# Performance work log

Measured on AMD Instinct MI355X. Metric: run time of the kernel, lower is better.

Reference implementation:

```python
import jax, jax.numpy as jnp
import numpy as np

N_NODES = 100000
N_EDGES = 3200000
NUM_GRAPHS = 2048
IN_CH = 35
HID = 128
EPS = 1e-5


def setup_inputs() -> dict:
    key = jax.random.key(0)
    ks = jax.random.split(key, 16)
    x = jax.random.normal(ks[0], (N_NODES, IN_CH), dtype=jnp.float32)
    edge_index = jax.random.randint(ks[1], (2, N_EDGES), 0, N_NODES, dtype=jnp.int64)
    batch = jnp.sort(jax.random.randint(ks[2], (N_NODES,), 0, NUM_GRAPHS, dtype=jnp.int64))
    def lin(k, fan_in, fan_out):
        b = 1.0 / np.sqrt(fan_in)
        kw, kb = jax.random.split(k)
        W = jax.random.uniform(kw, (fan_in, fan_out), minval=-b, maxval=b, dtype=jnp.float32)
        bias = jax.random.uniform(kb, (fan_out,), minval=-b, maxval=b, dtype=jnp.float32)
        return W, bias
    W1, b1 = lin(ks[3], IN_CH, HID)
    W2, b2 = lin(ks[4], HID, HID)
    W3, b3 = lin(ks[5], HID, HID)
    Wl1, bl1 = lin(ks[6], HID, HID // 2)
    Wl2, bl2 = lin(ks[7], HID // 2, 1)
    ones = jnp.ones((HID,), jnp.float32)
    zeros = jnp.zeros((HID,), jnp.float32)
    return {
        'x': x, 'edge_index': edge_index, 'batch': batch,
        'W1': W1, 'b1': b1, 'g1': ones, 'be1': zeros,
        'W2': W2, 'b2': b2, 'g2': ones, 'be2': zeros,
        'W3': W3, 'b3': b3, 'g3': ones, 'be3': zeros,
        'Wl1': Wl1, 'bl1': bl1, 'Wl2': Wl2, 'bl2': bl2,
    }


def _gcn_norm(edge_index, n):
    # add self-loops, compute symmetric normalization D^-1/2 (A+I) D^-1/2
    loop = jnp.arange(n, dtype=edge_index.dtype)
    src = jnp.concatenate([edge_index[0], loop])
    dst = jnp.concatenate([edge_index[1], loop])
    deg = jax.ops.segment_sum(jnp.ones_like(dst, jnp.float32), dst, num_segments=n)
    dinv = jnp.where(deg > 0, jax.lax.rsqrt(deg), 0.0)
    norm = dinv[src] * dinv[dst]
    return src, dst, norm


def _gcn_conv(x, src, dst, norm, W, b):
    h = x @ W                      # [N, out]
    msg = h[src] * norm[:, None]   # gather + scale (irregular)
    out = jax.ops.segment_sum(msg, dst, num_segments=x.shape[0])
    return out + b


def _bn(x, g, be):
    mu = jnp.mean(x, axis=0)
    var = jnp.mean(jnp.square(x - mu), axis=0)  # biased var (torch BN training)
    return (x - mu) * jax.lax.rsqrt(var + EPS) * g + be


def reference(x, edge_index, batch, W1, b1, g1, be1, W2, b2, g2, be2,
              W3, b3, g3, be3, Wl1, bl1, Wl2, bl2):
    n = x.shape[0]
    src, dst, norm = _gcn_norm(edge_index, n)
    h = jax.nn.gelu(_bn(_gcn_conv(x, src, dst, norm, W1, b1), g1, be1), approximate=False)
    h = jax.nn.gelu(_bn(_gcn_conv(h, src, dst, norm, W2, b2), g2, be2), approximate=False)
    h = jax.nn.gelu(_bn(_gcn_conv(h, src, dst, norm, W3, b3), g3, be3), approximate=False)
    # global mean pool by graph id
    s = jax.ops.segment_sum(h, batch, num_segments=NUM_GRAPHS)
    cnt = jax.ops.segment_sum(jnp.ones((n,), jnp.float32), batch, num_segments=NUM_GRAPHS)
    pooled = s / jnp.maximum(cnt, 1.0)[:, None]
    out = jax.nn.elu(pooled @ Wl1 + bl1)
    out = out @ Wl2 + bl2
    return out  # [NUM_GRAPHS, 1]
```

## Files before the change

### kernel.cpp

```cpp
#include <hip/hip_runtime.h>
#include <hip/hip_bf16.h>
#include <math.h>

#define N_NODES 100000
#define N_EDGES 3200000
#define NUM_GRAPHS 2048
#define IN_CH 35
#define HID 128
#define BN_EPS 1e-5f

#define BUCK_SHIFT 9
#define BUCK_SIZE 512
#define NB_BUCK 196
#define BUCK_CAP 18432
#define BIN_GRID 1024
#define BIN_CHUNK 3128

typedef short bf16x8 __attribute__((ext_vector_type(8)));
typedef float f32x4 __attribute__((ext_vector_type(4)));

__device__ __forceinline__ float gelu_f(float x) {
    return 0.5f * x * (1.0f + erff(x * 0.70710678118654752440f));
}

__device__ __forceinline__ float bflo(unsigned v) { return __uint_as_float(v << 16); }
__device__ __forceinline__ float bfhi(unsigned v) { return __uint_as_float(v & 0xffff0000u); }
__device__ __forceinline__ unsigned f2bf(float f) {
    unsigned x = __float_as_uint(f);
    return (x + 0x7fffu + ((x >> 16) & 1u)) >> 16;
}
__device__ __forceinline__ unsigned packbf2(float lo, float hi) {
    return f2bf(lo) | (f2bf(hi) << 16);
}


__global__ void k_zero2(int* __restrict__ gcnt, float* __restrict__ stats,
                        unsigned* __restrict__ xzero, unsigned* __restrict__ hzero) {
    int i = threadIdx.x;
    if (i < NB_BUCK) gcnt[i] = 0;
    if (i < 3 * 256) stats[i] = 0.0f;
    if (i < 32) xzero[i] = 0u;
    if (i < 64) hzero[i] = 0u;
}


__global__ void k_wcast(const float* __restrict__ W2, const float* __restrict__ W3,
                        unsigned* __restrict__ Wt2, unsigned* __restrict__ Wt3) {
    int t = blockIdx.x * 256 + threadIdx.x;
    if (t >= 2 * 8192) return;
    const float* W = (t < 8192) ? W2 : W3;
    unsigned* Wt = (t < 8192) ? Wt2 : Wt3;
    int i = t & 8191;
    int n = i >> 6, j = i & 63;
    Wt[n * 64 + j] = packbf2(W[(2 * j) * HID + n], W[(2 * j + 1) * HID + n]);
}


__global__ void k_bin(const int* __restrict__ ei, int* __restrict__ gcnt,
                      unsigned* __restrict__ epack) {
    __shared__ unsigned lpack[BIN_CHUNK];
    __shared__ unsigned char lbuck[BIN_CHUNK];
    __shared__ int hist[NB_BUCK];
    __shared__ int hbase[NB_BUCK];
    __shared__ int lcur[NB_BUCK];
    int tid = threadIdx.x;
    if (tid < NB_BUCK) { hist[tid] = 0; lcur[tid] = 0; }
    __syncthreads();
    int e0 = blockIdx.x * BIN_CHUNK;
    int nE = min(e0 + BIN_CHUNK, N_EDGES) - e0;
    for (int i = tid * 4; i < nE; i += 1024) {
        int4 s4 = *(const int4*)(ei + e0 + i);
        int4 d4 = *(const int4*)(ei + N_EDGES + e0 + i);
        lpack[i + 0] = (unsigned)s4.x | (((unsigned)d4.x & 511u) << 17);
        lpack[i + 1] = (unsigned)s4.y | (((unsigned)d4.y & 511u) << 17);
        lpack[i + 2] = (unsigned)s4.z | (((unsigned)d4.z & 511u) << 17);
        lpack[i + 3] = (unsigned)s4.w | (((unsigned)d4.w & 511u) << 17);
        int b0 = d4.x >> BUCK_SHIFT, b1 = d4.y >> BUCK_SHIFT;
        int b2 = d4.z >> BUCK_SHIFT, b3 = d4.w >> BUCK_SHIFT;
        lbuck[i + 0] = (unsigned char)b0;
        lbuck[i + 1] = (unsigned char)b1;
        lbuck[i + 2] = (unsigned char)b2;
        lbuck[i + 3] = (unsigned char)b3;
        atomicAdd(&hist[b0], 1);
        atomicAdd(&hist[b1], 1);
        atomicAdd(&hist[b2], 1);
        atomicAdd(&hist[b3], 1);
    }
    __syncthreads();
    if (tid < NB_BUCK) {
        int h = hist[tid];
        hbase[tid] = (h > 0) ? (tid * BUCK_CAP + atomicAdd(&gcnt[tid], h)) : 0;
    }
    __syncthreads();
    for (int i = tid; i < nE; i += 256) {
        int b = lbuck[i];
        int off = atomicAdd(&lcur[b], 1);
        epack[hbase[b] + off] = lpack[i];
    }
}


__global__ void k_fill(const int* __restrict__ gcnt, const unsigned* __restrict__ epack,
                       int* __restrict__ rowp, int* __restrict__ rowpEnd,
                       float* __restrict__ dinv, int* __restrict__ col) {
    __shared__ int ldeg[BUCK_SIZE];
    __shared__ int sa[BUCK_SIZE];
    __shared__ int sb[BUCK_SIZE];
    __shared__ int lcur[BUCK_SIZE];
    int b = blockIdx.x;
    int tid = threadIdx.x;
    int base_node = b << BUCK_SHIFT;
    int nn = min(BUCK_SIZE, N_NODES - base_node);
    int seg0 = b * BUCK_CAP;
    int seg1 = seg0 + gcnt[b];
    ldeg[tid] = 0;
    __syncthreads();
    for (int e = seg0 + tid; e < seg1; e += BUCK_SIZE) {
        atomicAdd(&ldeg[epack[e] >> 17], 1);
    }
    __syncthreads();
    sa[tid] = ldeg[tid];
    __syncthreads();
    int* src = sa; int* dst = sb;
    for (int st = 1; st < BUCK_SIZE; st <<= 1) {
        int v = src[tid];
        if (tid >= st) v += src[tid - st];
        dst[tid] = v;
        __syncthreads();
        int* t = src; src = dst; dst = t;
    }
    int ex = (tid == 0) ? 0 : src[tid - 1];
    int rp = seg0 + ex;
    lcur[tid] = rp;
    if (tid < nn) {
        rowp[base_node + tid] = rp;
        rowpEnd[base_node + tid] = rp + ldeg[tid];
        dinv[base_node + tid] = rsqrtf((float)(ldeg[tid] + 1));
    }
    __syncthreads();
    for (int e = seg0 + tid; e < seg1; e += BUCK_SIZE) {
        unsigned v = epack[e];
        int p = atomicAdd(&lcur[v >> 17], 1);
        col[p] = (int)(v & 0x1FFFFu);
    }
}


__global__ void k_castx(const float* __restrict__ X, const float* __restrict__ dinv,
                        unsigned* __restrict__ Xb) {
    int i = blockIdx.x * blockDim.x + threadIdx.x;
    if (i >= N_NODES * 32) return;
    int n = i >> 5, j = i & 31;
    float dv = dinv[n];
    float lo = 0.0f, hi = 0.0f;
    if (j < 17) {
        lo = X[(size_t)n * IN_CH + 2 * j];
        hi = X[(size_t)n * IN_CH + 2 * j + 1];
    } else if (j == 17) {
        lo = X[(size_t)n * IN_CH + 34];
    }
    Xb[i] = packbf2(dv * lo, dv * hi);
}

#define ACC8(v) { a0 += bflo(v.x); a1 += bfhi(v.x); a2 += bflo(v.y); a3 += bfhi(v.y); \
                  a4 += bflo(v.z); a5 += bfhi(v.z); a6 += bflo(v.w); a7 += bfhi(v.w); }
#define ACC4(v) { a0 += bflo(v.x); a1 += bfhi(v.x); a2 += bflo(v.y); a3 += bfhi(v.y); }


#define C1_NODES 8

__global__ __launch_bounds__(512) void k_conv1(
        const unsigned* __restrict__ Xb, const int* __restrict__ rowp,
        const int* __restrict__ rowpEnd, const int* __restrict__ col,
        const float* __restrict__ dinv,
        const float* __restrict__ W1, const float* __restrict__ b1,
        unsigned* __restrict__ Yb) {
    __shared__ float w_s[IN_CH * HID];
    __shared__ float b_s[HID];
    __shared__ float xa_s[C1_NODES][36];
    int tid = threadIdx.x;
    for (int u = tid; u < IN_CH * HID; u += 512) w_s[u] = W1[u];
    if (tid < HID) b_s[tid] = b1[tid];

    int wid = tid >> 6;
    int lane = tid & 63;
    int g = lane >> 4;
    int j = lane & 15;
    int node = blockIdx.x * C1_NODES + wid;
    bool valid = node < N_NODES;

    float a0 = 0.0f, a1 = 0.0f, a2 = 0.0f, a3 = 0.0f;
    float di = 0.0f;
    if (valid) {
        int rp0 = rowp[node], rp1 = rowpEnd[node];
        di = dinv[node];
        uint2 sv = *(const uint2*)(Xb + (size_t)node * 32 + j * 2);
        float w0 = (g == 0) ? 1.0f : 0.0f;
        a0 = w0 * bflo(sv.x); a1 = w0 * bfhi(sv.x);
        a2 = w0 * bflo(sv.y); a3 = w0 * bfhi(sv.y);
        unsigned deg = (unsigned)(rp1 - rp0);
        for (int e0 = (rp0 & ~3); e0 < rp1; e0 += 32) {
            int ebA = e0 + 4 * g;
            int ebB = ebA + 16;
            int4 cA = *(const int4*)(col + ebA);
            int4 cB = *(const int4*)(col + ebB);
            int s0 = ((unsigned)(ebA + 0 - rp0) < deg) ? cA.x : N_NODES;
            int s1 = ((unsigned)(ebA + 1 - rp0) < deg) ? cA.y : N_NODES;
            int s2 = ((unsigned)(ebA + 2 - rp0) < deg) ? cA.z : N_NODES;
            int s3 = ((unsigned)(ebA + 3 - rp0) < deg) ? cA.w : N_NODES;
            int s4 = ((unsigned)(ebB + 0 - rp0) < deg) ? cB.x : N_NODES;
            int s5 = ((unsigned)(ebB + 1 - rp0) < deg) ? cB.y : N_NODES;
            int s6 = ((unsigned)(ebB + 2 - rp0) < deg) ? cB.z : N_NODES;
            int s7 = ((unsigned)(ebB + 3 - rp0) < deg) ? cB.w : N_NODES;
            uint2 v0 = *(const uint2*)(Xb + (size_t)s0 * 32 + j * 2);
            uint2 v1 = *(const uint2*)(Xb + (size_t)s1 * 32 + j * 2);
            uint2 v2 = *(const uint2*)(Xb + (size_t)s2 * 32 + j * 2);
            uint2 v3 = *(const uint2*)(Xb + (size_t)s3 * 32 + j * 2);
            uint2 v4 = *(const uint2*)(Xb + (size_t)s4 * 32 + j * 2);
            uint2 v5 = *(const uint2*)(Xb + (size_t)s5 * 32 + j * 2);
            uint2 v6 = *(const uint2*)(Xb + (size_t)s6 * 32 + j * 2);
            uint2 v7 = *(const uint2*)(Xb + (size_t)s7 * 32 + j * 2);
            ACC4(v0); ACC4(v1); ACC4(v2); ACC4(v3);
            ACC4(v4); ACC4(v5); ACC4(v6); ACC4(v7);
        }
    }
    a0 += __shfl(a0, (lane + 32) & 63, 64);
    a1 += __shfl(a1, (lane + 32) & 63, 64);
    a2 += __shfl(a2, (lane + 32) & 63, 64);
    a3 += __shfl(a3, (lane + 32) & 63, 64);
    a0 += __shfl(a0, (lane + 16) & 63, 64);
    a1 += __shfl(a1, (lane + 16) & 63, 64);
    a2 += __shfl(a2, (lane + 16) & 63, 64);
    a3 += __shfl(a3, (lane + 16) & 63, 64);
    if (valid && g == 0 && j < 9) {
        xa_s[wid][4 * j + 0] = di * a0;
        xa_s[wid][4 * j + 1] = di * a1;
        xa_s[wid][4 * j + 2] = di * a2;
        xa_s[wid][4 * j + 3] = di * a3;
    }
    __syncthreads();
    float acc0 = b_s[2 * lane];
    float acc1 = b_s[2 * lane + 1];
    #pragma unroll 7
    for (int k = 0; k < IN_CH; ++k) {
        float xv = xa_s[wid][k];
        acc0 = fmaf(xv, w_s[k * HID + 2 * lane], acc0);
        acc1 = fmaf(xv, w_s[k * HID + 2 * lane + 1], acc1);
    }
    if (valid) Yb[(size_t)node * 64 + lane] = packbf2(acc0, acc1);
}


__global__ __launch_bounds__(256) void k_gemm128m(
        const unsigned* __restrict__ Yb, const float* __restrict__ stats,
        const float* __restrict__ g, const float* __restrict__ be,
        const unsigned* __restrict__ Wt, const float* __restrict__ dinv,
        unsigned* __restrict__ Hb) {
    __shared__ __align__(16) unsigned act[64 * 64];
    __shared__ float sc_s[HID];
    __shared__ float sh_s[HID];
    int tid = threadIdx.x;
    if (tid < HID) {
        const float inv_n = 1.0f / (float)N_NODES;
        float mean = stats[tid] * inv_n;
        float var = stats[HID + tid] * inv_n - mean * mean;
        float s = g[tid] * rsqrtf(var + BN_EPS);
        sc_s[tid] = s;
        sh_s[tid] = be[tid] - mean * s;
    }
    __syncthreads();
    int row0 = blockIdx.x * 64;
    #pragma unroll
    for (int it = 0; it < 8; ++it) {
        int idx = it * 256 + tid;
        int r = idx >> 5;
        int c2 = idx & 31;
        int gr = row0 + r;
        uint2 v = make_uint2(0u, 0u);
        if (gr < N_NODES) v = *(const uint2*)(Yb + (size_t)gr * 64 + c2 * 2);
        int c = c2 * 2;
        float x0 = gelu_f(fmaf(bflo(v.x), sc_s[2 * c], sh_s[2 * c]));
        float x1 = gelu_f(fmaf(bfhi(v.x), sc_s[2 * c + 1], sh_s[2 * c + 1]));
        float x2 = gelu_f(fmaf(bflo(v.y), sc_s[2 * c + 2], sh_s[2 * c + 2]));
        float x3 = gelu_f(fmaf(bfhi(v.y), sc_s[2 * c + 3], sh_s[2 * c + 3]));
        int swz = (r & 7) << 2;
        act[r * 64 + (c ^ swz)]       = packbf2(x0, x1);
        act[r * 64 + ((c + 1) ^ swz)] = packbf2(x2, x3);
    }
    __syncthreads();
    int l = tid & 63;
    int w = tid >> 6;
    int r0 = w * 16;
    int arow = r0 + (l & 15);
    int kgrp = l >> 4;
    bf16x8 afrag[4];
    #pragma unroll
    for (int kk = 0; kk < 4; ++kk) {
        int base = (kk * 16 + kgrp * 4) ^ ((arow & 7) << 2);
        afrag[kk] = *(const bf16x8*)&act[arow * 64 + base];
    }
    float dv[4];
    #pragma unroll
    for (int reg = 0; reg < 4; ++reg) {
        int gr = row0 + r0 + kgrp * 4 + reg;
        dv[reg] = (gr < N_NODES) ? dinv[gr] : 0.0f;
    }
    unsigned short* Hb16 = (unsigned short*)Hb;
    #pragma unroll
    for (int n0 = 0; n0 < 8; ++n0) {
        f32x4 acc = {0.0f, 0.0f, 0.0f, 0.0f};
        #pragma unroll
        for (int kk = 0; kk < 4; ++kk) {
            bf16x8 b = *(const bf16x8*)&Wt[(n0 * 16 + (l & 15)) * 64 + kk * 16 + kgrp * 4];
            acc = __builtin_amdgcn_mfma_f32_16x16x32_bf16(afrag[kk], b, acc, 0, 0, 0);
        }
        int colg = n0 * 16 + (l & 15);
        #pragma unroll
        for (int reg = 0; reg < 4; ++reg) {
            int gr = row0 + r0 + kgrp * 4 + reg;
            if (gr < N_NODES)
                Hb16[(size_t)gr * HID + colg] = (unsigned short)f2bf(dv[reg] * acc[reg]);
        }
    }
}


__global__ void k_convb(const unsigned* __restrict__ Hb, const int* __restrict__ rowp,
                        const int* __restrict__ rowpEnd, const int* __restrict__ col,
                        const float* __restrict__ dinv,
                        const float* __restrict__ bias, unsigned* __restrict__ Yb) {
    int tid = threadIdx.x;
    int wid = tid >> 6;
    int lane = tid & 63;
    int g = lane >> 4;
    int j = lane & 15;
    int node = blockIdx.x * 4 + wid;
    if (node >= N_NODES) return;
    int rp0 = rowp[node], rp1 = rowpEnd[node];
    float di = dinv[node];
    uint4 sv = *(const uint4*)(Hb + (size_t)node * 64 + j * 4);
    float w0 = (g == 0) ? 1.0f : 0.0f;
    float a0 = w0 * bflo(sv.x), a1 = w0 * bfhi(sv.x);
    float a2 = w0 * bflo(sv.y), a3 = w0 * bfhi(sv.y);
    float a4 = w0 * bflo(sv.z), a5 = w0 * bfhi(sv.z);
    float a6 = w0 * bflo(sv.w), a7 = w0 * bfhi(sv.w);
    unsigned deg = (unsigned)(rp1 - rp0);
    for (int e0 = (rp0 & ~3); e0 < rp1; e0 += 32) {
        int ebA = e0 + 4 * g;
        int ebB = ebA + 16;
        int4 cA = *(const int4*)(col + ebA);
        int4 cB = *(const int4*)(col + ebB);
        int s0 = ((unsigned)(ebA + 0 - rp0) < deg) ? cA.x : N_NODES;
        int s1 = ((unsigned)(ebA + 1 - rp0) < deg) ? cA.y : N_NODES;
        int s2 = ((unsigned)(ebA + 2 - rp0) < deg) ? cA.z : N_NODES;
        int s3 = ((unsigned)(ebA + 3 - rp0) < deg) ? cA.w : N_NODES;
        int s4 = ((unsigned)(ebB + 0 - rp0) < deg) ? cB.x : N_NODES;
        int s5 = ((unsigned)(ebB + 1 - rp0) < deg) ? cB.y : N_NODES;
        int s6 = ((unsigned)(ebB + 2 - rp0) < deg) ? cB.z : N_NODES;
        int s7 = ((unsigned)(ebB + 3 - rp0) < deg) ? cB.w : N_NODES;
        uint4 v0 = *(const uint4*)(Hb + (size_t)s0 * 64 + j * 4);
        uint4 v1 = *(const uint4*)(Hb + (size_t)s1 * 64 + j * 4);
        uint4 v2 = *(const uint4*)(Hb + (size_t)s2 * 64 + j * 4);
        uint4 v3 = *(const uint4*)(Hb + (size_t)s3 * 64 + j * 4);
        uint4 v4 = *(const uint4*)(Hb + (size_t)s4 * 64 + j * 4);
        uint4 v5 = *(const uint4*)(Hb + (size_t)s5 * 64 + j * 4);
        uint4 v6 = *(const uint4*)(Hb + (size_t)s6 * 64 + j * 4);
        uint4 v7 = *(const uint4*)(Hb + (size_t)s7 * 64 + j * 4);
        ACC8(v0); ACC8(v1); ACC8(v2); ACC8(v3);
        ACC8(v4); ACC8(v5); ACC8(v6); ACC8(v7);
    }
    a0 += __shfl(a0, (lane + 32) & 63, 64);
    a1 += __shfl(a1, (lane + 32) & 63, 64);
    a2 += __shfl(a2, (lane + 32) & 63, 64);
    a3 += __shfl(a3, (lane + 32) & 63, 64);
    a4 += __shfl(a4, (lane + 32) & 63, 64);
    a5 += __shfl(a5, (lane + 32) & 63, 64);
    a6 += __shfl(a6, (lane + 32) & 63, 64);
    a7 += __shfl(a7, (lane + 32) & 63, 64);
    a0 += __shfl(a0, (lane + 16) & 63, 64);
    a1 += __shfl(a1, (lane + 16) & 63, 64);
    a2 += __shfl(a2, (lane + 16) & 63, 64);
    a3 += __shfl(a3, (lane + 16) & 63, 64);
    a4 += __shfl(a4, (lane + 16) & 63, 64);
    a5 += __shfl(a5, (lane + 16) & 63, 64);
    a6 += __shfl(a6, (lane + 16) & 63, 64);
    a7 += __shfl(a7, (lane + 16) & 63, 64);
    if (g == 0) {
        const float4* bp = (const float4*)(bias + 8 * j);
        float4 bA = bp[0], bB = bp[1];
        uint4 o;
        o.x = packbf2(fmaf(di, a0, bA.x), fmaf(di, a1, bA.y));
        o.y = packbf2(fmaf(di, a2, bA.z), fmaf(di, a3, bA.w));
        o.z = packbf2(fmaf(di, a4, bB.x), fmaf(di, a5, bB.y));
        o.w = packbf2(fmaf(di, a6, bB.z), fmaf(di, a7, bB.w));
        *(uint4*)(Yb + (size_t)node * 64 + j * 4) = o;
    }
}


__global__ void k_statsb(const unsigned* __restrict__ Yb, float* __restrict__ stats) {
    __shared__ float red[16][128];
    __shared__ float red2[16][128];
    int tid = threadIdx.x;
    int j = tid & 15;
    int rg = tid >> 4;
    float s[8] = {0, 0, 0, 0, 0, 0, 0, 0};
    float q[8] = {0, 0, 0, 0, 0, 0, 0, 0};
    for (int r = blockIdx.x * 16 + rg; r < N_NODES; r += gridDim.x * 16) {
        uint4 v = *(const uint4*)(Yb + (size_t)r * 64 + j * 4);
        float x;
        x = bflo(v.x); s[0] += x; q[0] = fmaf(x, x, q[0]);
        x = bfhi(v.x); s[1] += x; q[1] = fmaf(x, x, q[1]);
        x = bflo(v.y); s[2] += x; q[2] = fmaf(x, x, q[2]);
        x = bfhi(v.y); s[3] += x; q[3] = fmaf(x, x, q[3]);
        x = bflo(v.z); s[4] += x; q[4] = fmaf(x, x, q[4]);
        x = bfhi(v.z); s[5] += x; q[5] = fmaf(x, x, q[5]);
        x = bflo(v.w); s[6] += x; q[6] = fmaf(x, x, q[6]);
        x = bfhi(v.w); s[7] += x; q[7] = fmaf(x, x, q[7]);
    }
    #pragma unroll
    for (int k = 0; k < 8; ++k) {
        red[rg][8 * j + k]  = s[k];
        red2[rg][8 * j + k] = q[k];
    }
    __syncthreads();
    if (tid < 128) {
        float S = 0.0f, Q = 0.0f;
        #pragma unroll
        for (int r = 0; r < 16; ++r) { S += red[r][tid]; Q += red2[r][tid]; }
        atomicAdd(&stats[tid], S);
        atomicAdd(&stats[128 + tid], Q);
    }
}


__device__ __forceinline__ int lowerb(const int* __restrict__ arr, int n, int key) {
    int lo = 0, hi = n;
    while (lo < hi) {
        int mid = (lo + hi) >> 1;
        if (arr[mid] < key) lo = mid + 1; else hi = mid;
    }
    return lo;
}

__global__ void k_pool_mlp(const unsigned* __restrict__ Yb, const float* __restrict__ stats,
                           const float* __restrict__ g, const float* __restrict__ be,
                           const int* __restrict__ batch,
                           const float* __restrict__ Wl1, const float* __restrict__ bl1,
                           const float* __restrict__ Wl2, const float* __restrict__ bl2,
                           float* __restrict__ out) {
    __shared__ float pooled[128];
    __shared__ float part[2][128];
    __shared__ float sc_s[128];
    __shared__ float sh_s[128];
    __shared__ int bounds[2];
    int gidx = blockIdx.x;
    int tid = threadIdx.x;
    if (tid < 128) {
        const float inv_n = 1.0f / (float)N_NODES;
        float mean = stats[tid] * inv_n;
        float var = stats[128 + tid] * inv_n - mean * mean;
        float s = g[tid] * rsqrtf(var + BN_EPS);
        sc_s[tid] = s;
        sh_s[tid] = be[tid] - mean * s;
    }
    if (tid == 0) {
        bounds[0] = lowerb(batch, N_NODES, gidx);
        bounds[1] = lowerb(batch, N_NODES, gidx + 1);
    }
    __syncthreads();
    int lo = bounds[0], hi = bounds[1];
    int rofs = tid >> 6;
    int w = tid & 63;
    float sA = sc_s[2 * w], hA = sh_s[2 * w];
    float sB = sc_s[2 * w + 1], hB = sh_s[2 * w + 1];
    float accA = 0.0f, accB = 0.0f;
    for (int r = lo + rofs; r < hi; r += 2) {
        unsigned v = Yb[(size_t)r * 64 + w];
        accA += gelu_f(fmaf(bflo(v), sA, hA));
        accB += gelu_f(fmaf(bfhi(v), sB, hB));
    }
    part[rofs][2 * w]     = accA;
    part[rofs][2 * w + 1] = accB;
    __syncthreads();
    if (tid < 128)
        pooled[tid] = (hi > lo) ? (part[0][tid] + part[1][tid]) / (float)(hi - lo) : 0.0f;
    __syncthreads();
    if (tid < 64) {
        float hs = bl1[tid];
        #pragma unroll 4
        for (int k = 0; k < 128; ++k)
            hs = fmaf(pooled[k], Wl1[k * 64 + tid], hs);
        float e = (hs > 0.0f) ? hs : expm1f(hs);
        float pv = e * Wl2[tid];
        #pragma unroll
        for (int o = 32; o > 0; o >>= 1)
            pv += __shfl_down(pv, o);
        if (tid == 0) out[gidx] = pv + bl2[0];
    }
}


extern "C" void kernel_launch(void* const* d_in, const int* in_sizes, int n_in,
                              void* d_out, int out_size, void* d_ws, size_t ws_size,
                              hipStream_t stream) {
    const float* x   = (const float*)d_in[0];
    const int*   ei  = (const int*)d_in[1];
    const int*   bat = (const int*)d_in[2];
    const float* W1  = (const float*)d_in[3];
    const float* b1  = (const float*)d_in[4];
    const float* g1  = (const float*)d_in[5];
    const float* be1 = (const float*)d_in[6];
    const float* W2  = (const float*)d_in[7];
    const float* b2  = (const float*)d_in[8];
    const float* g2  = (const float*)d_in[9];
    const float* be2 = (const float*)d_in[10];
    const float* W3  = (const float*)d_in[11];
    const float* b3  = (const float*)d_in[12];
    const float* g3  = (const float*)d_in[13];
    const float* be3 = (const float*)d_in[14];
    const float* Wl1 = (const float*)d_in[15];
    const float* bl1 = (const float*)d_in[16];
    const float* Wl2 = (const float*)d_in[17];
    const float* bl2 = (const float*)d_in[18];
    float* out = (float*)d_out;

    char* ws = (char*)d_ws;
    size_t off = 0;
    auto alloc = [&](size_t bytes) -> char* {
        char* p = ws + off;
        off += (bytes + 255) & ~(size_t)255;
        return p;
    };
    int*      gcnt    = (int*)alloc(NB_BUCK * sizeof(int));
    unsigned* epack   = (unsigned*)alloc(((size_t)NB_BUCK * BUCK_CAP + 64) * sizeof(unsigned));
    int*      rowp    = (int*)alloc(N_NODES * sizeof(int));
    int*      rowpEnd = (int*)alloc(N_NODES * sizeof(int));
    float*    dinv    = (float*)alloc(N_NODES * sizeof(float));
    int*      col     = (int*)alloc(((size_t)NB_BUCK * BUCK_CAP + 64) * sizeof(int));
    unsigned* Xb      = (unsigned*)alloc((size_t)(N_NODES + 1) * 32 * sizeof(unsigned));
    unsigned* Ybuf    = (unsigned*)alloc((size_t)N_NODES * 64 * sizeof(unsigned));
    unsigned* Hbuf    = (unsigned*)alloc((size_t)(N_NODES + 1) * 64 * sizeof(unsigned));
    float*    stats   = (float*)alloc(3 * 256 * sizeof(float));
    unsigned* Wt2     = (unsigned*)alloc(8192 * sizeof(unsigned));
    unsigned* Wt3     = (unsigned*)alloc(8192 * sizeof(unsigned));

    k_zero2<<<1, 1024, 0, stream>>>(gcnt, stats, Xb + (size_t)N_NODES * 32,
                                    Hbuf + (size_t)N_NODES * 64);
    k_wcast<<<64, 256, 0, stream>>>(W2, W3, Wt2, Wt3);
    k_bin<<<BIN_GRID, 256, 0, stream>>>(ei, gcnt, epack);
    k_fill<<<NB_BUCK, BUCK_SIZE, 0, stream>>>(gcnt, epack, rowp, rowpEnd, dinv, col);
    k_castx<<<(N_NODES * 32 + 255) / 256, 256, 0, stream>>>(x, dinv, Xb);

    const int gemm_blocks = (N_NODES + 63) / 64;
    const int conv_blocks = (N_NODES + 3) / 4;

    k_conv1<<<(N_NODES + C1_NODES - 1) / C1_NODES, 512, 0, stream>>>(
        Xb, rowp, rowpEnd, col, dinv, W1, b1, Ybuf);
    k_statsb<<<1024, 256, 0, stream>>>(Ybuf, stats + 0 * 256);

    k_gemm128m<<<gemm_blocks, 256, 0, stream>>>(Ybuf, stats + 0 * 256, g1, be1, Wt2, dinv, Hbuf);
    k_convb<<<conv_blocks, 256, 0, stream>>>(Hbuf, rowp, rowpEnd, col, dinv, b2, Ybuf);
    k_statsb<<<1024, 256, 0, stream>>>(Ybuf, stats + 1 * 256);

    k_gemm128m<<<gemm_blocks, 256, 0, stream>>>(Ybuf, stats + 1 * 256, g2, be2, Wt3, dinv, Hbuf);
    k_convb<<<conv_blocks, 256, 0, stream>>>(Hbuf, rowp, rowpEnd, col, dinv, b3, Ybuf);
    k_statsb<<<1024, 256, 0, stream>>>(Ybuf, stats + 2 * 256);

    k_pool_mlp<<<NUM_GRAPHS, 128, 0, stream>>>(Ybuf, stats + 2 * 256, g3, be3, bat,
                                               Wl1, bl1, Wl2, bl2, out);
}
```

Measured before the change: 677.5 us.

## Fuse BatchNorm statistics into conv kernels with slotted atomics and finalize kernel

Removes the separate k_statsb passes by accumulating per-channel sum and sum-of-squares inside k_conv1 and k_convb. Each block reduces in shared memory and atomically adds into one of 128 partial slots. A small k_statfin kernel folds the slots into the BN scale and shift, which the gemm and pool kernels now read directly. The zero and weight-cast kernels are merged into one init launch. The aim is to avoid re-reading the 25MB activation buffer three times; the cost is extra shared-memory traffic and global atomics in the conv kernels, plus stats computed from fp32 values before bf16 rounding.

```diff
diff --git a/kernel.cpp b/kernel.cpp
--- a/kernel.cpp
+++ b/kernel.cpp
@@ -15,6 +15,7 @@
 #define BUCK_CAP 18432
 #define BIN_GRID 1024
 #define BIN_CHUNK 3128
+#define NSLOT 128
 
 typedef short bf16x8 __attribute__((ext_vector_type(8)));
 typedef float f32x4 __attribute__((ext_vector_type(4)));
@@ -34,25 +35,26 @@
 }
 
 
-__global__ void k_zero2(int* __restrict__ gcnt, float* __restrict__ stats,
-                        unsigned* __restrict__ xzero, unsigned* __restrict__ hzero) {
-    int i = threadIdx.x;
-    if (i < NB_BUCK) gcnt[i] = 0;
-    if (i < 3 * 256) stats[i] = 0.0f;
-    if (i < 32) xzero[i] = 0u;
-    if (i < 64) hzero[i] = 0u;
-}
-
-
-__global__ void k_wcast(const float* __restrict__ W2, const float* __restrict__ W3,
-                        unsigned* __restrict__ Wt2, unsigned* __restrict__ Wt3) {
-    int t = blockIdx.x * 256 + threadIdx.x;
-    if (t >= 2 * 8192) return;
-    const float* W = (t < 8192) ? W2 : W3;
-    unsigned* Wt = (t < 8192) ? Wt2 : Wt3;
-    int i = t & 8191;
-    int n = i >> 6, j = i & 63;
-    Wt[n * 64 + j] = packbf2(W[(2 * j) * HID + n], W[(2 * j + 1) * HID + n]);
+__global__ void k_init(int* __restrict__ gcnt, float* __restrict__ pstat,
+                       unsigned* __restrict__ xzero, unsigned* __restrict__ hzero,
+                       const float* __restrict__ W2, const float* __restrict__ W3,
+                       unsigned* __restrict__ Wt2, unsigned* __restrict__ Wt3) {
+    int b = blockIdx.x;
+    if (b < 64) {
+        int t = b * 256 + threadIdx.x;
+        const float* W = (t < 8192) ? W2 : W3;
+        unsigned* Wt = (t < 8192) ? Wt2 : Wt3;
+        int i = t & 8191;
+        int n = i >> 6, j = i & 63;
+        Wt[n * 64 + j] = packbf2(W[(2 * j) * HID + n], W[(2 * j + 1) * HID + n]);
+    } else if (b < 64 + 3 * NSLOT) {
+        pstat[(size_t)(b - 64) * 256 + threadIdx.x] = 0.0f;
+    } else {
+        int i = threadIdx.x;
+        if (i < NB_BUCK) gcnt[i] = 0;
+        if (i < 32) xzero[i] = 0u;
+        if (i < 64) hzero[i] = 0u;
+    }
 }
 
 
@@ -115,9 +117,8 @@
     int seg1 = seg0 + gcnt[b];
     ldeg[tid] = 0;
     __syncthreads();
-    for (int e = seg0 + tid; e < seg1; e += BUCK_SIZE) {
+    for (int e = seg0 + tid; e < seg1; e += BUCK_SIZE)
         atomicAdd(&ldeg[epack[e] >> 17], 1);
-    }
     __syncthreads();
     sa[tid] = ldeg[tid];
     __syncthreads();
@@ -174,10 +175,11 @@
         const int* __restrict__ rowpEnd, const int* __restrict__ col,
         const float* __restrict__ dinv,
         const float* __restrict__ W1, const float* __restrict__ b1,
-        unsigned* __restrict__ Yb) {
+        unsigned* __restrict__ Yb, float* __restrict__ pstat) {
     __shared__ float w_s[IN_CH * HID];
     __shared__ float b_s[HID];
     __shared__ float xa_s[C1_NODES][36];
+    __shared__ float lsum[C1_NODES][256];
     int tid = threadIdx.x;
     for (int u = tid; u < IN_CH * HID; u += 512) w_s[u] = W1[u];
     if (tid < HID) b_s[tid] = b1[tid];
@@ -248,12 +250,45 @@
         acc1 = fmaf(xv, w_s[k * HID + 2 * lane + 1], acc1);
     }
     if (valid) Yb[(size_t)node * 64 + lane] = packbf2(acc0, acc1);
+    lsum[wid][2 * lane]           = acc0;
+    lsum[wid][2 * lane + 1]       = acc1;
+    lsum[wid][128 + 2 * lane]     = acc0 * acc0;
+    lsum[wid][128 + 2 * lane + 1] = acc1 * acc1;
+    __syncthreads();
+    if (tid < 256) {
+        float v = 0.0f;
+        #pragma unroll
+        for (int wv = 0; wv < C1_NODES; ++wv) v += lsum[wv][tid];
+        atomicAdd(&pstat[(size_t)(blockIdx.x & (NSLOT - 1)) * 256 + tid], v);
+    }
+}
+
+
+__global__ void k_statfin(const float* __restrict__ pstat, const float* __restrict__ g,
+                          const float* __restrict__ be, float* __restrict__ scsh) {
+    __shared__ float red[4][256];
+    int tid = threadIdx.x;
+    int c = tid & 255;
+    int grp = tid >> 8;
+    float S = 0.0f;
+    for (int s = grp; s < NSLOT; s += 4) S += pstat[(size_t)s * 256 + c];
+    red[grp][c] = S;
+    __syncthreads();
+    if (tid < 128) {
+        float Ssum = red[0][tid] + red[1][tid] + red[2][tid] + red[3][tid];
+        float Qsum = red[0][128 + tid] + red[1][128 + tid] + red[2][128 + tid] + red[3][128 + tid];
+        const float inv_n = 1.0f / (float)N_NODES;
+        float mean = Ssum * inv_n;
+        float var = Qsum * inv_n - mean * mean;
+        float sc = g[tid] * rsqrtf(var + BN_EPS);
+        scsh[tid] = sc;
+        scsh[128 + tid] = be[tid] - mean * sc;
+    }
 }
 
 
 __global__ __launch_bounds__(256) void k_gemm128m(
-        const unsigned* __restrict__ Yb, const float* __restrict__ stats,
-        const float* __restrict__ g, const float* __restrict__ be,
+        const unsigned* __restrict__ Yb, const float* __restrict__ scsh,
         const unsigned* __restrict__ Wt, const float* __restrict__ dinv,
         unsigned* __restrict__ Hb) {
     __shared__ __align__(16) unsigned act[64 * 64];
@@ -261,12 +296,8 @@
     __shared__ float sh_s[HID];
     int tid = threadIdx.x;
     if (tid < HID) {
-        const float inv_n = 1.0f / (float)N_NODES;
-        float mean = stats[tid] * inv_n;
-        float var = stats[HID + tid] * inv_n - mean * mean;
-        float s = g[tid] * rsqrtf(var + BN_EPS);
-        sc_s[tid] = s;
-        sh_s[tid] = be[tid] - mean * s;
+        sc_s[tid] = scsh[tid];
+        sh_s[tid] = scsh[128 + tid];
     }
     __syncthreads();
     int row0 = blockIdx.x * 64;
@@ -328,14 +359,19 @@
 __global__ void k_convb(const unsigned* __restrict__ Hb, const int* __restrict__ rowp,
                         const int* __restrict__ rowpEnd, const int* __restrict__ col,
                         const float* __restrict__ dinv,
-                        const float* __restrict__ bias, unsigned* __restrict__ Yb) {
+                        const float* __restrict__ bias, unsigned* __restrict__ Yb,
+                        float* __restrict__ pstat) {
+    __shared__ float lsum[4][256];
     int tid = threadIdx.x;
     int wid = tid >> 6;
     int lane = tid & 63;
     int g = lane >> 4;
     int j = lane & 15;
     int node = blockIdx.x * 4 + wid;
-    if (node >= N_NODES) return;
+    if (tid < 256) { lsum[tid >> 6][(tid & 63) * 4 + 0] = 0.0f; }
+    #pragma unroll
+    for (int z = 0; z < 4; ++z) ((float*)lsum)[z * 256 + tid] = 0.0f;
+    __syncthreads();
     int rp0 = rowp[node], rp1 = rowpEnd[node];
     float di = dinv[node];
     uint4 sv = *(const uint4*)(Hb + (size_t)node * 64 + j * 4);
@@ -369,67 +405,38 @@
         ACC8(v0); ACC8(v1); ACC8(v2); ACC8(v3);
         ACC8(v4); ACC8(v5); ACC8(v6); ACC8(v7);
     }
-    a0 += __shfl(a0, (lane + 32) & 63, 64);
-    a1 += __shfl(a1, (lane + 32) & 63, 64);
-    a2 += __shfl(a2, (lane + 32) & 63, 64);
-    a3 += __shfl(a3, (lane + 32) & 63, 64);
-    a4 += __shfl(a4, (lane + 32) & 63, 64);
-    a5 += __shfl(a5, (lane + 32) & 63, 64);
-    a6 += __shfl(a6, (lane + 32) & 63, 64);
-    a7 += __shfl(a7, (lane + 32) & 63, 64);
-    a0 += __shfl(a0, (lane + 16) & 63, 64);
-    a1 += __shfl(a1, (lane + 16) & 63, 64);
-    a2 += __shfl(a2, (lane + 16) & 63, 64);
-    a3 += __shfl(a3, (lane + 16) & 63, 64);
-    a4 += __shfl(a4, (lane + 16) & 63, 64);
-    a5 += __shfl(a5, (lane + 16) & 63, 64);
-    a6 += __shfl(a6, (lane + 16) & 63, 64);
-    a7 += __shfl(a7, (lane + 16) & 63, 64);
+    #define RED(o) { a0 += __shfl(a0,(lane+o)&63,64); a1 += __shfl(a1,(lane+o)&63,64); \
+                     a2 += __shfl(a2,(lane+o)&63,64); a3 += __shfl(a3,(lane+o)&63,64); \
+                     a4 += __shfl(a4,(lane+o)&63,64); a5 += __shfl(a5,(lane+o)&63,64); \
+                     a6 += __shfl(a6,(lane+o)&63,64); a7 += __shfl(a7,(lane+o)&63,64); }
+    RED(32); RED(16);
+    #undef RED
     if (g == 0) {
         const float4* bp = (const float4*)(bias + 8 * j);
         float4 bA = bp[0], bB = bp[1];
+        float y0 = fmaf(di, a0, bA.x), y1 = fmaf(di, a1, bA.y);
+        float y2 = fmaf(di, a2, bA.z), y3 = fmaf(di, a3, bA.w);
+        float y4 = fmaf(di, a4, bB.x), y5 = fmaf(di, a5, bB.y);
+        float y6 = fmaf(di, a6, bB.z), y7 = fmaf(di, a7, bB.w);
         uint4 o;
-        o.x = packbf2(fmaf(di, a0, bA.x), fmaf(di, a1, bA.y));
-        o.y = packbf2(fmaf(di, a2, bA.z), fmaf(di, a3, bA.w));
-        o.z = packbf2(fmaf(di, a4, bB.x), fmaf(di, a5, bB.y));
-        o.w = packbf2(fmaf(di, a6, bB.z), fmaf(di, a7, bB.w));
+        o.x = packbf2(y0, y1);
+        o.y = packbf2(y2, y3);
+        o.z = packbf2(y4, y5);
+        o.w = packbf2(y6, y7);
         *(uint4*)(Yb + (size_t)node * 64 + j * 4) = o;
-    }
-}
-
-
-__global__ void k_statsb(const unsigned* __restrict__ Yb, float* __restrict__ stats) {
-    __shared__ float red[16][128];
-    __shared__ float red2[16][128];
-    int tid = threadIdx.x;
-    int j = tid & 15;
-    int rg = tid >> 4;
-    float s[8] = {0, 0, 0, 0, 0, 0, 0, 0};
-    float q[8] = {0, 0, 0, 0, 0, 0, 0, 0};
-    for (int r = blockIdx.x * 16 + rg; r < N_NODES; r += gridDim.x * 16) {
-        uint4 v = *(const uint4*)(Yb + (size_t)r * 64 + j * 4);
-        float x;
-        x = bflo(v.x); s[0] += x; q[0] = fmaf(x, x, q[0]);
-        x = bfhi(v.x); s[1] += x; q[1] = fmaf(x, x, q[1]);
-        x = bflo(v.y); s[2] += x; q[2] = fmaf(x, x, q[2]);
-        x = bfhi(v.y); s[3] += x; q[3] = fmaf(x, x, q[3]);
-        x = bflo(v.z); s[4] += x; q[4] = fmaf(x, x, q[4]);
-        x = bfhi(v.z); s[5] += x; q[5] = fmaf(x, x, q[5]);
-        x = bflo(v.w); s[6] += x; q[6] = fmaf(x, x, q[6]);
-        x = bfhi(v.w); s[7] += x; q[7] = fmaf(x, x, q[7]);
-    }
-    #pragma unroll
-    for (int k = 0; k < 8; ++k) {
-        red[rg][8 * j + k]  = s[k];
-        red2[rg][8 * j + k] = q[k];
-    }
-    __syncthreads();
-    if (tid < 128) {
-        float S = 0.0f, Q = 0.0f;
-        #pragma unroll
-        for (int r = 0; r < 16; ++r) { S += red[r][tid]; Q += red2[r][tid]; }
-        atomicAdd(&stats[tid], S);
-        atomicAdd(&stats[128 + tid], Q);
+        lsum[wid][8 * j + 0] = y0; lsum[wid][8 * j + 1] = y1;
+        lsum[wid][8 * j + 2] = y2; lsum[wid][8 * j + 3] = y3;
+        lsum[wid][8 * j + 4] = y4; lsum[wid][8 * j + 5] = y5;
+        lsum[wid][8 * j + 6] = y6; lsum[wid][8 * j + 7] = y7;
+        lsum[wid][128 + 8 * j + 0] = y0 * y0; lsum[wid][128 + 8 * j + 1] = y1 * y1;
+        lsum[wid][128 + 8 * j + 2] = y2 * y2; lsum[wid][128 + 8 * j + 3] = y3 * y3;
+        lsum[wid][128 + 8 * j + 4] = y4 * y4; lsum[wid][128 + 8 * j + 5] = y5 * y5;
+        lsum[wid][128 + 8 * j + 6] = y6 * y6; lsum[wid][128 + 8 * j + 7] = y7 * y7;
+    }
+    __syncthreads();
+    if (tid < 256) {
+        float v = lsum[0][tid] + lsum[1][tid] + lsum[2][tid] + lsum[3][tid];
+        atomicAdd(&pstat[(size_t)(blockIdx.x & (NSLOT - 1)) * 256 + tid], v);
     }
 }
 
@@ -443,8 +450,7 @@
     return lo;
 }
 
-__global__ void k_pool_mlp(const unsigned* __restrict__ Yb, const float* __restrict__ stats,
-                           const float* __restrict__ g, const float* __restrict__ be,
+__global__ void k_pool_mlp(const unsigned* __restrict__ Yb, const float* __restrict__ scsh,
                            const int* __restrict__ batch,
                            const float* __restrict__ Wl1, const float* __restrict__ bl1,
                            const float* __restrict__ Wl2, const float* __restrict__ bl2,
@@ -457,12 +463,8 @@
     int gidx = blockIdx.x;
     int tid = threadIdx.x;
     if (tid < 128) {
-        const float inv_n = 1.0f / (float)N_NODES;
-        float mean = stats[tid] * inv_n;
-        float var = stats[128 + tid] * inv_n - mean * mean;
-        float s = g[tid] * rsqrtf(var + BN_EPS);
-        sc_s[tid] = s;
-        sh_s[tid] = be[tid] - mean * s;
+        sc_s[tid] = scsh[tid];
+        sh_s[tid] = scsh[128 + tid];
     }
     if (tid == 0) {
         bounds[0] = lowerb(batch, N_NODES, gidx);
@@ -541,32 +543,34 @@
     unsigned* Xb      = (unsigned*)alloc((size_t)(N_NODES + 1) * 32 * sizeof(unsigned));
     unsigned* Ybuf    = (unsigned*)alloc((size_t)N_NODES * 64 * sizeof(unsigned));
     unsigned* Hbuf    = (unsigned*)alloc((size_t)(N_NODES + 1) * 64 * sizeof(unsigned));
-    float*    stats   = (float*)alloc(3 * 256 * sizeof(float));
+    float*    pstat   = (float*)alloc((size_t)3 * NSLOT * 256 * sizeof(float));
+    float*    scsh    = (float*)alloc(3 * 256 * sizeof(float));
     unsigned* Wt2     = (unsigned*)alloc(8192 * sizeof(unsigned));
     unsigned* Wt3     = (unsigned*)alloc(8192 * sizeof(unsigned));
 
-    k_zero2<<<1, 1024, 0, stream>>>(gcnt, stats, Xb + (size_t)N_NODES * 32,
-                                    Hbuf + (size_t)N_NODES * 64);
-    k_wcast<<<64, 256, 0, stream>>>(W2, W3, Wt2, Wt3);
+    k_init<<<64 + 3 * NSLOT + 1, 256, 0, stream>>>(gcnt, pstat, Xb + (size_t)N_NODES * 32,
+                                                   Hbuf + (size_t)N_NODES * 64, W2, W3, Wt2, Wt3);
     k_bin<<<BIN_GRID, 256, 0, stream>>>(ei, gcnt, epack);
     k_fill<<<NB_BUCK, BUCK_SIZE, 0, stream>>>(gcnt, epack, rowp, rowpEnd, dinv, col);
     k_castx<<<(N_NODES * 32 + 255) / 256, 256, 0, stream>>>(x, dinv, Xb);
 
     const int gemm_blocks = (N_NODES + 63) / 64;
-    const int conv_blocks = (N_NODES + 3) / 4;
-
-    k_conv1<<<(N_NODES + C1_NODES - 1) / C1_NODES, 512, 0, stream>>>(
-        Xb, rowp, rowpEnd, col, dinv, W1, b1, Ybuf);
-    k_statsb<<<1024, 256, 0, stream>>>(Ybuf, stats + 0 * 256);
-
-    k_gemm128m<<<gemm_blocks, 256, 0, stream>>>(Ybuf, stats + 0 * 256, g1, be1, Wt2, dinv, Hbuf);
-    k_convb<<<conv_blocks, 256, 0, stream>>>(Hbuf, rowp, rowpEnd, col, dinv, b2, Ybuf);
-    k_statsb<<<1024, 256, 0, stream>>>(Ybuf, stats + 1 * 256);
-
-    k_gemm128m<<<gemm_blocks, 256, 0, stream>>>(Ybuf, stats + 1 * 256, g2, be2, Wt3, dinv, Hbuf);
-    k_convb<<<conv_blocks, 256, 0, stream>>>(Hbuf, rowp, rowpEnd, col, dinv, b3, Ybuf);
-    k_statsb<<<1024, 256, 0, stream>>>(Ybuf, stats + 2 * 256);
-
-    k_pool_mlp<<<NUM_GRAPHS, 128, 0, stream>>>(Ybuf, stats + 2 * 256, g3, be3, bat,
+    const int conv_blocks = N_NODES / 4;
+
+    k_conv1<<<N_NODES / C1_NODES, 512, 0, stream>>>(
+        Xb, rowp, rowpEnd, col, dinv, W1, b1, Ybuf, pstat + 0 * NSLOT * 256);
+    k_statfin<<<1, 1024, 0, stream>>>(pstat + 0 * NSLOT * 256, g1, be1, scsh + 0 * 256);
+
+    k_gemm128m<<<gemm_blocks, 256, 0, stream>>>(Ybuf, scsh + 0 * 256, Wt2, dinv, Hbuf);
+    k_convb<<<conv_blocks, 256, 0, stream>>>(Hbuf, rowp, rowpEnd, col, dinv, b2, Ybuf,
+                                             pstat + 1 * NSLOT * 256);
+    k_statfin<<<1, 1024, 0, stream>>>(pstat + 1 * NSLOT * 256, g2, be2, scsh + 1 * 256);
+
+    k_gemm128m<<<gemm_blocks, 256, 0, stream>>>(Ybuf, scsh + 1 * 256, Wt3, dinv, Hbuf);
+    k_convb<<<conv_blocks, 256, 0, stream>>>(Hbuf, rowp, rowpEnd, col, dinv, b3, Ybuf,
+                                             pstat + 2 * NSLOT * 256);
+    k_statfin<<<1, 1024, 0, stream>>>(pstat + 2 * NSLOT * 256, g3, be3, scsh + 2 * 256);
+
+    k_pool_mlp<<<NUM_GRAPHS, 128, 0, stream>>>(Ybuf, scsh + 2 * 256, bat,
                                                Wl1, bl1, Wl2, bl2, out);
 }
```

After: 635.2 us. 6.2% less time.
